# Kernel tuning notes

Hardware: AMD Instinct MI355X
Metric: run time of the kernel (lower is better)

Reference implementation:

```python
import math
import jax, jax.numpy as jnp
import numpy as np

R = 15  # static Gaussian truncation radius (covers 3*sigma for resolutions up to ~12)
SIG_PER_FWHM = 1.0 / math.sqrt(8.0 * math.log(2.0))  # sigma = fwhm / sqrt(8 ln 2)


def _blur_resample_axis0(img, sigma, res):
    """Gaussian blur (dct2/symmetric boundary) + down/up resize along axis 0.

    img: [H, W]; sigma, res: scalars. anchor='f' resize convention:
      down (factor=1/res): low coord j samples input at j*res
      up   (factor=res, shape=H): out coord i samples low grid at i/res
    Low-res grid has n_low = max(floor(H/res), 1) valid rows; positions are
    clamped to the valid range (edge boundary).
    """
    H, W = img.shape
    dt = img.dtype
    # --- separable 1D Gaussian blur along axis 0 ---
    off = jnp.arange(-R, R + 1, dtype=dt)
    sig = jnp.maximum(sigma, jnp.asarray(1e-6, dt))
    w = jnp.exp(-0.5 * (off / sig) ** 2)
    w = w / w.sum()
    pad = jnp.pad(img, ((R, R), (0, 0)), mode='symmetric')  # dct2 boundary
    s = w[0] * pad[0:H]
    for k in range(1, 2 * R + 1):
        s = s + w[k] * pad[k:k + H]
    # --- downsample (factor = 1/res, anchor 'f') ---
    Hf = jnp.asarray(H, dt)
    n_low = jnp.maximum(jnp.floor(Hf / res), 1.0).astype(jnp.int32)
    pos = jnp.clip(jnp.arange(H, dtype=dt) * res, 0.0, Hf - 1.0)
    lo = jnp.floor(pos)
    fr = (pos - lo)[:, None]
    lo_i = lo.astype(jnp.int32)
    hi_i = jnp.minimum(lo_i + 1, H - 1)
    low = s[lo_i] * (1.0 - fr) + s[hi_i] * fr  # [H, W], rows >= n_low unused
    # --- upsample back to H (factor = res, anchor 'f') ---
    pos2 = jnp.clip(jnp.arange(H, dtype=dt) / res, 0.0, n_low.astype(dt) - 1.0)
    lo2 = jnp.floor(pos2)
    fr2 = (pos2 - lo2)[:, None]
    lo2_i = jnp.minimum(lo2.astype(jnp.int32), n_low - 1)
    hi2_i = jnp.minimum(lo2_i + 1, n_low - 1)
    return low[lo2_i] * (1.0 - fr2) + low[hi2_i] * fr2


def _process_one(img, res, ax, gp):
    fwhm = res * gp
    sigma = fwhm * SIG_PER_FWHM
    out0 = _blur_resample_axis0(img, sigma, res)          # degrade axis 0 (H)
    out1 = _blur_resample_axis0(img.T, sigma, res).T      # degrade axis 1 (W)
    return jnp.where(ax == 0, out0, out1)


def setup_inputs() -> dict:
    key = jax.random.key(0)
    k_x, k_res, k_ax, k_gap = jax.random.split(key, 4)
    B, C, H, W = 16, 4, 512, 512
    x = jax.random.normal(k_x, (B, C, H, W), dtype=jnp.float32)
    # lognormal with mean 3, sd 3 -> underlying normal params
    m, sdev = 3.0, 3.0
    var_log = math.log(1.0 + (sdev / m) ** 2)
    mu = math.log(m) - 0.5 * var_log
    z = jax.random.normal(k_res, (B, C), dtype=jnp.float32)
    resolution = jnp.clip(jnp.exp(mu + math.sqrt(var_log) * z), 1.0, None)
    axis = jax.random.randint(k_ax, (B, C), 0, 2, dtype=jnp.int32)
    gap = jax.random.uniform(k_gap, (B, C), dtype=jnp.float32)
    return {"x": x, "resolution": resolution, "axis": axis, "gap": gap}


def reference(x, resolution, axis, gap):
    B, C, H, W = x.shape
    flat = x.reshape(B * C, H, W)
    out = jax.vmap(_process_one)(flat, resolution.reshape(-1), axis.reshape(-1), gap.reshape(-1))
    return out.reshape(B, C, H, W)
```

## Files before the change

kernel.cpp:

```cpp
#include <hip/hip_runtime.h>
#include <math.h>


#define RR 15
#define TAPS 31
#define SEG0 8
#define SIG_PER_FWHM 0.42466090014400953f

__global__ __launch_bounds__(256) void lowres2d_kernel(
    const float* __restrict__ x,
    const float* __restrict__ resolution,
    const int*   __restrict__ axis,
    const float* __restrict__ gap,
    float* __restrict__ out)
{
    const int tid = threadIdx.x;
    const int n   = blockIdx.y;
    const int bx  = blockIdx.x;

    const float res = resolution[n];
    const int   ax  = axis[n];
    const float gp  = gap[n];

    if (ax == 0 && bx >= 64) return;

    const float sig = fmaxf(res * gp * SIG_PER_FWHM, 1e-6f);
    int n_low = (int)floorf(512.0f / res);
    if (n_low < 1) n_low = 1;
    if (n_low > 512) n_low = 512;
    const float nlm1f = (float)(n_low - 1);

    int kr = (int)(sig * 5.2565f) + 1;
    if (kr > RR) kr = RR;
    const int k0 = RR - kr, k1 = RR + 1 + kr;
    const int la_lo = kr, la_hi = 510 - kr;

    __shared__ float we[34];
    __shared__ float dwe[32];
    __shared__ float s_img[4][520];
    __shared__ float s_low[4][516];

    if (tid < 32) {
        const int k = tid;
        float r = 0.0f;
        if (k < TAPS) {
            float d = (float)(k - RR) / sig;
            r = expf(-0.5f * d * d);
        }
        float tot = r;
        tot += __shfl_xor(tot, 1, 32);
        tot += __shfl_xor(tot, 2, 32);
        tot += __shfl_xor(tot, 4, 32);
        tot += __shfl_xor(tot, 8, 32);
        tot += __shfl_xor(tot, 16, 32);
        float rm1 = __shfl_up(r, 1, 32);
        if (k == 0) rm1 = 0.0f;
        const float inv = 1.0f / tot;
        we[k + 1] = r * inv;
        if (k == 0) we[0] = 0.0f;
        dwe[k] = (rm1 - r) * inv;
    }
    __syncthreads();

    const size_t base = (size_t)n * (512 * 512);
    const float* img = x + base;
    float* o = out + base;

    if (ax == 0) {
        const int v2  = tid;
        const int i0  = bx * SEG0;
        const float2* img2 = (const float2*)img;
        float2* out2 = (float2*)o;

        auto compute_low = [&](int j) -> float2 {
            float pos = fminf((float)j * res, 511.0f);
            float lof = floorf(pos);
            float fr  = pos - lof;
            int   la  = (int)lof;
            float2 acc = make_float2(0.0f, 0.0f);
            if (la >= la_lo && la <= la_hi) {
                #pragma unroll 4
                for (int k = k0; k <= k1; ++k) {
                    int t = la - RR + k;
                    float cw = fmaf(fr, dwe[k], we[k + 1]);
                    float2 val = img2[(size_t)(t * 256 + v2)];
                    acc.x = fmaf(cw, val.x, acc.x);
                    acc.y = fmaf(cw, val.y, acc.y);
                }
            } else {
                for (int k = k0; k <= k1; ++k) {
                    int t = la - RR + k;
                    t = (t < 0)   ? (-1 - t)   : t;
                    t = (t > 511) ? (1023 - t) : t;
                    float cw = fmaf(fr, dwe[k], we[k + 1]);
                    float2 val = img2[(size_t)(t * 256 + v2)];
                    acc.x = fmaf(cw, val.x, acc.x);
                    acc.y = fmaf(cw, val.y, acc.y);
                }
            }
            return acc;
        };

        float p0 = fminf((float)i0 / res, nlm1f);
        int j = (int)floorf(p0);
        if (j > n_low - 1) j = n_low - 1;
        float2 lowA = compute_low(j);
        int jB = (j + 1 < n_low) ? (j + 1) : (n_low - 1);
        float2 lowB = (jB == j) ? lowA : compute_low(jB);

        for (int i = i0; i < i0 + SEG0; ++i) {
            float pos2 = fminf((float)i / res, nlm1f);
            float l2f  = floorf(pos2);
            float fr2  = pos2 - l2f;
            int lo2 = (int)l2f;
            if (lo2 > n_low - 1) lo2 = n_low - 1;

            if (lo2 == j + 1) {
                j = lo2;
                lowA = lowB;
                jB = (j + 1 < n_low) ? (j + 1) : (n_low - 1);
                lowB = (jB == j) ? lowA : compute_low(jB);
            } else if (lo2 > j + 1) {
                j = lo2;
                lowA = compute_low(j);
                jB = (j + 1 < n_low) ? (j + 1) : (n_low - 1);
                lowB = (jB == j) ? lowA : compute_low(jB);
            }
            float omf2 = 1.0f - fr2;
            out2[(size_t)(i * 256 + v2)] =
                make_float2(lowA.x * omf2 + lowB.x * fr2,
                            lowA.y * omf2 + lowB.y * fr2);
        }
    } else {
        const int h0 = bx * 4;

        const float4* img4 = (const float4*)(img + (size_t)h0 * 512);
        #pragma unroll
        for (int p = 0; p < 2; ++p) {
            int m = p * 256 + tid;
            int r = m >> 7, c4 = m & 127;
            ((float4*)&s_img[r][0])[c4] = img4[r * 128 + c4];
        }
        __syncthreads();

        {
            const int r = tid >> 6;
            for (int j = (tid & 63); j < n_low; j += 64) {
                float pos = fminf((float)j * res, 511.0f);
                float lof = floorf(pos);
                float fr  = pos - lof;
                int   la  = (int)lof;
                float acc = 0.0f;
                if (la >= la_lo && la <= la_hi) {
                    #pragma unroll 4
                    for (int k = k0; k <= k1; ++k) {
                        int t = la - RR + k;
                        float cw = fmaf(fr, dwe[k], we[k + 1]);
                        acc = fmaf(cw, s_img[r][t], acc);
                    }
                } else {
                    for (int k = k0; k <= k1; ++k) {
                        int t = la - RR + k;
                        t = (t < 0)   ? (-1 - t)   : t;
                        t = (t > 511) ? (1023 - t) : t;
                        float cw = fmaf(fr, dwe[k], we[k + 1]);
                        acc = fmaf(cw, s_img[r][t], acc);
                    }
                }
                s_low[r][j] = acc;
            }
        }
        __syncthreads();

        float4* out4 = (float4*)(o + (size_t)h0 * 512);
        #pragma unroll
        for (int p = 0; p < 2; ++p) {
            int m = p * 256 + tid;
            int r = m >> 7, c4 = m & 127;
            float vals[4];
            #pragma unroll
            for (int q = 0; q < 4; ++q) {
                int i = c4 * 4 + q;
                float pos2 = fminf((float)i / res, nlm1f);
                float l2f  = floorf(pos2);
                float fr2  = pos2 - l2f;
                int lo2 = (int)l2f;
                if (lo2 > n_low - 1) lo2 = n_low - 1;
                int hi2 = (lo2 + 1 < n_low) ? (lo2 + 1) : (n_low - 1);
                vals[q] = s_low[r][lo2] * (1.0f - fr2) + s_low[r][hi2] * fr2;
            }
            float4 ov;
            ov.x = vals[0]; ov.y = vals[1]; ov.z = vals[2]; ov.w = vals[3];
            out4[r * 128 + c4] = ov;
        }
    }
}

extern "C" void kernel_launch(void* const* d_in, const int* in_sizes, int n_in,
                              void* d_out, int out_size, void* d_ws, size_t ws_size,
                              hipStream_t stream) {
    const float* x          = (const float*)d_in[0];
    const float* resolution = (const float*)d_in[1];
    const int*   axis       = (const int*)d_in[2];
    const float* gap        = (const float*)d_in[3];
    float* out = (float*)d_out;

    const int n_img = in_sizes[1];

    dim3 grid(128, n_img);
    lowres2d_kernel<<<grid, 256, 0, stream>>>(x, resolution, axis, gap, out);
}
```

Baseline: 132.7 us.

## Cooperatively compute axis-0 low-res rows into shared memory with float4 loads

Measured after the change: 136.2 us. 1.03x slower.

```diff
diff --git a/kernel.cpp b/kernel.cpp
--- a/kernel.cpp
+++ b/kernel.cpp
@@ -5,6 +5,7 @@
 #define RR 15
 #define TAPS 31
 #define SEG0 8
+#define MAXJ 10
 #define SIG_PER_FWHM 0.42466090014400953f
 
 __global__ __launch_bounds__(256) void lowres2d_kernel(
@@ -37,8 +38,7 @@
 
     __shared__ float we[34];
     __shared__ float dwe[32];
-    __shared__ float s_img[4][520];
-    __shared__ float s_low[4][516];
+    __shared__ float smem[MAXJ * 512];
 
     if (tid < 32) {
         const int k = tid;
@@ -67,25 +67,34 @@
     float* o = out + base;
 
     if (ax == 0) {
-        const int v2  = tid;
-        const int i0  = bx * SEG0;
-        const float2* img2 = (const float2*)img;
-        float2* out2 = (float2*)o;
-
-        auto compute_low = [&](int j) -> float2 {
+        const int i0 = bx * SEG0;
+        const float4* img4 = (const float4*)img;
+
+        int jA = (int)floorf(fminf((float)i0 / res, nlm1f));
+        if (jA > n_low - 1) jA = n_low - 1;
+        int jL = (int)floorf(fminf((float)(i0 + SEG0 - 1) / res, nlm1f));
+        if (jL > n_low - 1) jL = n_low - 1;
+        int jB = (jL + 1 < n_low) ? (jL + 1) : (n_low - 1);
+        const int mlow = jB - jA + 1;
+
+        for (int it = tid; it < mlow * 128; it += 256) {
+            const int c4 = it & 127;
+            const int jj = it >> 7;
+            const int j  = jA + jj;
             float pos = fminf((float)j * res, 511.0f);
             float lof = floorf(pos);
             float fr  = pos - lof;
             int   la  = (int)lof;
-            float2 acc = make_float2(0.0f, 0.0f);
+            float4 acc = make_float4(0.0f, 0.0f, 0.0f, 0.0f);
             if (la >= la_lo && la <= la_hi) {
-                #pragma unroll 4
                 for (int k = k0; k <= k1; ++k) {
                     int t = la - RR + k;
                     float cw = fmaf(fr, dwe[k], we[k + 1]);
-                    float2 val = img2[(size_t)(t * 256 + v2)];
-                    acc.x = fmaf(cw, val.x, acc.x);
-                    acc.y = fmaf(cw, val.y, acc.y);
+                    float4 v = img4[(size_t)(t * 128 + c4)];
+                    acc.x = fmaf(cw, v.x, acc.x);
+                    acc.y = fmaf(cw, v.y, acc.y);
+                    acc.z = fmaf(cw, v.z, acc.z);
+                    acc.w = fmaf(cw, v.w, acc.w);
                 }
             } else {
                 for (int k = k0; k <= k1; ++k) {
@@ -93,58 +102,58 @@
                     t = (t < 0)   ? (-1 - t)   : t;
                     t = (t > 511) ? (1023 - t) : t;
                     float cw = fmaf(fr, dwe[k], we[k + 1]);
-                    float2 val = img2[(size_t)(t * 256 + v2)];
-                    acc.x = fmaf(cw, val.x, acc.x);
-                    acc.y = fmaf(cw, val.y, acc.y);
+                    float4 v = img4[(size_t)(t * 128 + c4)];
+                    acc.x = fmaf(cw, v.x, acc.x);
+                    acc.y = fmaf(cw, v.y, acc.y);
+                    acc.z = fmaf(cw, v.z, acc.z);
+                    acc.w = fmaf(cw, v.w, acc.w);
                 }
             }
-            return acc;
-        };
-
-        float p0 = fminf((float)i0 / res, nlm1f);
-        int j = (int)floorf(p0);
-        if (j > n_low - 1) j = n_low - 1;
-        float2 lowA = compute_low(j);
-        int jB = (j + 1 < n_low) ? (j + 1) : (n_low - 1);
-        float2 lowB = (jB == j) ? lowA : compute_low(jB);
-
-        for (int i = i0; i < i0 + SEG0; ++i) {
-            float pos2 = fminf((float)i / res, nlm1f);
-            float l2f  = floorf(pos2);
-            float fr2  = pos2 - l2f;
-            int lo2 = (int)l2f;
-            if (lo2 > n_low - 1) lo2 = n_low - 1;
-
-            if (lo2 == j + 1) {
-                j = lo2;
-                lowA = lowB;
-                jB = (j + 1 < n_low) ? (j + 1) : (n_low - 1);
-                lowB = (jB == j) ? lowA : compute_low(jB);
-            } else if (lo2 > j + 1) {
-                j = lo2;
-                lowA = compute_low(j);
-                jB = (j + 1 < n_low) ? (j + 1) : (n_low - 1);
-                lowB = (jB == j) ? lowA : compute_low(jB);
-            }
-            float omf2 = 1.0f - fr2;
-            out2[(size_t)(i * 256 + v2)] =
-                make_float2(lowA.x * omf2 + lowB.x * fr2,
-                            lowA.y * omf2 + lowB.y * fr2);
+            ((float4*)(smem + jj * 512))[c4] = acc;
+        }
+        __syncthreads();
+
+        {
+            const int c4   = tid & 127;
+            const int half = tid >> 7;
+            float4* out4 = (float4*)o;
+            #pragma unroll
+            for (int q = 0; q < 4; ++q) {
+                const int i = i0 + half * 4 + q;
+                float pos2 = fminf((float)i / res, nlm1f);
+                float l2f  = floorf(pos2);
+                float fr2  = pos2 - l2f;
+                int lo2 = (int)l2f;
+                if (lo2 > n_low - 1) lo2 = n_low - 1;
+                int hi2 = (lo2 + 1 < n_low) ? (lo2 + 1) : (n_low - 1);
+                float4 a = ((const float4*)(smem + (lo2 - jA) * 512))[c4];
+                float4 b = ((const float4*)(smem + (hi2 - jA) * 512))[c4];
+                float om = 1.0f - fr2;
+                float4 ov;
+                ov.x = a.x * om + b.x * fr2;
+                ov.y = a.y * om + b.y * fr2;
+                ov.z = a.z * om + b.z * fr2;
+                ov.w = a.w * om + b.w * fr2;
+                out4[(size_t)(i * 128 + c4)] = ov;
+            }
         }
     } else {
         const int h0 = bx * 4;
+        float* s_img = smem;
+        float* s_low = smem + 4 * 520;
 
         const float4* img4 = (const float4*)(img + (size_t)h0 * 512);
         #pragma unroll
         for (int p = 0; p < 2; ++p) {
             int m = p * 256 + tid;
             int r = m >> 7, c4 = m & 127;
-            ((float4*)&s_img[r][0])[c4] = img4[r * 128 + c4];
+            ((float4*)(s_img + r * 520))[c4] = img4[r * 128 + c4];
         }
         __syncthreads();
 
         {
             const int r = tid >> 6;
+            const float* srow = s_img + r * 520;
             for (int j = (tid & 63); j < n_low; j += 64) {
                 float pos = fminf((float)j * res, 511.0f);
                 float lof = floorf(pos);
@@ -156,7 +165,7 @@
                     for (int k = k0; k <= k1; ++k) {
                         int t = la - RR + k;
                         float cw = fmaf(fr, dwe[k], we[k + 1]);
-                        acc = fmaf(cw, s_img[r][t], acc);
+                        acc = fmaf(cw, srow[t], acc);
                     }
                 } else {
                     for (int k = k0; k <= k1; ++k) {
@@ -164,10 +173,10 @@
                         t = (t < 0)   ? (-1 - t)   : t;
                         t = (t > 511) ? (1023 - t) : t;
                         float cw = fmaf(fr, dwe[k], we[k + 1]);
-                        acc = fmaf(cw, s_img[r][t], acc);
+                        acc = fmaf(cw, srow[t], acc);
                     }
                 }
-                s_low[r][j] = acc;
+                s_low[r * 516 + j] = acc;
             }
         }
         __syncthreads();
@@ -177,6 +186,7 @@
         for (int p = 0; p < 2; ++p) {
             int m = p * 256 + tid;
             int r = m >> 7, c4 = m & 127;
+            const float* lrow = s_low + r * 516;
             float vals[4];
             #pragma unroll
             for (int q = 0; q < 4; ++q) {
@@ -187,7 +197,7 @@
                 int lo2 = (int)l2f;
                 if (lo2 > n_low - 1) lo2 = n_low - 1;
                 int hi2 = (lo2 + 1 < n_low) ? (lo2 + 1) : (n_low - 1);
-                vals[q] = s_low[r][lo2] * (1.0f - fr2) + s_low[r][hi2] * fr2;
+                vals[q] = lrow[lo2] * (1.0f - fr2) + lrow[hi2] * fr2;
             }
             float4 ov;
             ov.x = vals[0]; ov.y = vals[1]; ov.z = vals[2]; ov.w = vals[3];
```
